# Kernel tuning notes

Hardware: AMD Instinct MI355X
Metric: run time of the kernel (lower is better)

The kernel has to match this reference:

```python
import jax, jax.numpy as jnp
import numpy as np

# Model dims (mamba-2.8b-ish layer, single 8192-token prefill)
H, I, N, R, K, L = 2048, 4096, 16, 128, 4, 8192


def setup_inputs() -> dict:
    key = jax.random.key(0)
    ks = jax.random.split(key, 7)
    return {
        "hidden_states": jax.random.normal(ks[0], (L, H), jnp.float32),
        "W_in": jax.random.normal(ks[1], (H, 2 * I), jnp.float32) * 0.02,   # in_proj (no bias)
        "conv_w": jax.random.normal(ks[2], (I, K), jnp.float32) * 0.2,      # depthwise conv weight
        "conv_b": jnp.zeros((I,), jnp.float32),                              # use_conv_bias=True
        "W_x": jax.random.normal(ks[3], (I, R + 2 * N), jnp.float32) * 0.02, # x_proj (no bias)
        "W_dt": jax.random.normal(ks[4], (R, I), jnp.float32) * 0.01,        # dt_proj weight
        "dt_bias": jax.random.normal(ks[5], (I,), jnp.float32) * 0.1,        # dt_proj bias (delta_bias)
        "A_log": jnp.log(jnp.broadcast_to(jnp.arange(1, N + 1, dtype=jnp.float32), (I, N))) + 0.0,
        "D": jnp.ones((I,), jnp.float32),
        "W_out": jax.random.normal(ks[6], (I, H), jnp.float32) * 0.02,       # out_proj (no bias)
    }


def silu(x):
    return x * jax.nn.sigmoid(x)


def causal_dw_conv(x, w, b):
    # x: [L, I]; depthwise causal conv along time (padding K-1, left only)
    xt = x.T[None]  # [1, I, L] (NCW)
    y = jax.lax.conv_general_dilated(xt, w[:, None, :], (1,), [(K - 1, 0)],
                                     feature_group_count=I)  # [1, I, L]
    return y[0].T + b


def mamba_forward(hidden_states, W_in, conv_w, conv_b, W_x, W_dt, dt_bias, A_log, D, W_out):
    proj = hidden_states @ W_in                     # [L, 2I]
    x, gate = proj[:, :I], proj[:, I:]
    x = silu(causal_dw_conv(x, conv_w, conv_b))     # causal_conv1d_fn with silu
    ssm = x @ W_x                                   # [L, R+2N]
    dt_lr, B, C = ssm[:, :R], ssm[:, R:R + N], ssm[:, R + N:]
    delta = jax.nn.softplus(dt_lr @ W_dt + dt_bias) # delta_softplus=True with delta_bias
    A = -jnp.exp(A_log)                             # [I, N]

    def step(h, t):
        d_t, B_t, C_t, u_t = t                      # [I], [N], [N], [I]
        h = h * jnp.exp(d_t[:, None] * A) + (d_t * u_t)[:, None] * B_t[None, :]
        return h, h @ C_t                           # y_t: [I]

    h0 = jnp.zeros((I, N), jnp.float32)
    _, y = jax.lax.scan(step, h0, (delta, B, C, x)) # y: [L, I]
    y = (y + x * D) * silu(gate)                    # skip D*u and z-gating (selective_scan_fn)
    return y @ W_out                                # out_proj -> [L, H]


def reference(hidden_states, W_in, conv_w, conv_b, W_x, W_dt, dt_bias, A_log, D, W_out):
    return mamba_forward(hidden_states, W_in, conv_w, conv_b, W_x, W_dt, dt_bias, A_log, D, W_out)
```

## Files before the change

### kernel.cpp

```cpp
#include <hip/hip_runtime.h>
#include <cmath>
#include <stdint.h>

#define H_DIM 2048
#define I_DIM 4096
#define N_DIM 16
#define R_DIM 128
#define K_CONV 4
#define L_DIM 8192
#define LC 2048
#define NCHUNK (L_DIM / LC)
#define SEG 32
#define TSEG (LC / SEG)
#define IN_DIM (I_DIM * N_DIM)

typedef _Float16 f16x8 __attribute__((ext_vector_type(8)));
typedef _Float16 f16x4v __attribute__((ext_vector_type(4)));
typedef float    f32x4 __attribute__((ext_vector_type(4)));

__device__ __forceinline__ void gl_lds(const _Float16* g, _Float16* lbase, int lane) {
#if __has_builtin(__builtin_amdgcn_global_load_lds)
    __builtin_amdgcn_global_load_lds(
        (const __attribute__((address_space(1))) void*)g,
        (__attribute__((address_space(3))) void*)lbase, 16, 0, 0);
#else
    *(f16x8*)&lbase[lane * 8] = *(const f16x8*)g;
#endif
}

template <int OUTF16>
__global__ __launch_bounds__(512, 1) void gemm_p256(
    const _Float16* __restrict__ Aph,
    const _Float16* __restrict__ Bph,
    void* __restrict__ Cv, int ldc, int Kd, int gm,
    int kchunk, size_t partStride)
{
    __shared__ __align__(16) _Float16 Sh[3][2][8192];

    const int tid = threadIdx.x;
    int bid = blockIdx.x;
    const int q = gridDim.x >> 3;
    bid = (bid & 7) * q + (bid >> 3);
    const int m0 = (bid % gm) * 256;
    const int n0 = (bid / gm) * 256;

    const int kbeg = blockIdx.y * kchunk;

    const int w = tid >> 6, l = tid & 63;
    const int wm = w & 3, wn = w >> 2;
    const int lr = l & 15, lg = l >> 4;

    const int KP = Kd >> 5;
    const int np0 = n0 >> 4, mp0 = m0 >> 4;
    const int st0 = w;

    f32x4 acc[4][8];
#pragma unroll
    for (int a = 0; a < 4; ++a)
#pragma unroll
        for (int b = 0; b < 8; ++b) acc[a][b] = (f32x4){0.f, 0.f, 0.f, 0.f};

    auto stage = [&](int k0, int p) {
        const int kp = k0 >> 5;
#pragma unroll
        for (int s = 0; s < 2; ++s) {
            const int st = st0 + s * 8;
            gl_lds(Aph + ((size_t)(mp0 + st) * KP + kp) * 512 + (size_t)l * 8,
                   &Sh[p][0][st * 512], l);
            gl_lds(Bph + ((size_t)(np0 + st) * KP + kp) * 512 + (size_t)l * 8,
                   &Sh[p][1][st * 512], l);
        }
    };
    auto domfma = [&](int b) {
        f16x8 fah[4];
#pragma unroll
        for (int t = 0; t < 4; ++t)
            fah[t] = *(const f16x8*)&Sh[b][0][(wm * 4 + t) * 512 + l * 8];
        __builtin_amdgcn_s_setprio(1);
#pragma unroll
        for (int nh = 0; nh < 2; ++nh) {
            f16x8 fbh[4];
#pragma unroll
            for (int t = 0; t < 4; ++t)
                fbh[t] = *(const f16x8*)&Sh[b][1][(wn * 8 + nh * 4 + t) * 512 + l * 8];
#pragma unroll
            for (int mt = 0; mt < 4; ++mt)
#pragma unroll
                for (int nt = 0; nt < 4; ++nt)
                    acc[mt][nh * 4 + nt] = __builtin_amdgcn_mfma_f32_16x16x32_f16(
                        fah[mt], fbh[nt], acc[mt][nh * 4 + nt], 0, 0, 0);
        }
        __builtin_amdgcn_s_setprio(0);
    };

    const int KT = kchunk >> 5;
    stage(kbeg, 0);
    stage(kbeg + 32, 1);
    for (int k = 0; k + 2 < KT; ++k) {
        stage(kbeg + (k + 2) * 32, (k + 2) % 3);
        asm volatile("s_waitcnt vmcnt(8)" ::: "memory");
        __builtin_amdgcn_s_barrier();
        __builtin_amdgcn_sched_barrier(0);
        domfma(k % 3);
        __builtin_amdgcn_s_barrier();
    }
    asm volatile("s_waitcnt vmcnt(4)" ::: "memory");
    __builtin_amdgcn_s_barrier();
    __builtin_amdgcn_sched_barrier(0);
    domfma((KT - 2) % 3);
    __builtin_amdgcn_s_barrier();
    asm volatile("s_waitcnt vmcnt(0)" ::: "memory");
    __builtin_amdgcn_s_barrier();
    __builtin_amdgcn_sched_barrier(0);
    domfma((KT - 1) % 3);

#pragma unroll
    for (int mt = 0; mt < 4; ++mt) {
        const int row = m0 + wm * 64 + mt * 16 + lg * 4;
#pragma unroll
        for (int nt = 0; nt < 8; ++nt) {
            const int col = n0 + wn * 128 + nt * 16 + lr;
#pragma unroll
            for (int j = 0; j < 4; ++j) {
                if (OUTF16) {
                    _Float16* C = (_Float16*)Cv + (size_t)blockIdx.y * partStride;
                    C[(size_t)(row + j) * ldc + col] = (_Float16)acc[mt][nt][j];
                } else {
                    float* C = (float*)Cv + (size_t)blockIdx.y * partStride;
                    C[(size_t)(row + j) * ldc + col] = acc[mt][nt][j];
                }
            }
        }
    }
}

__global__ __launch_bounds__(256) void reduce4_f16_kernel(
    const _Float16* __restrict__ P, float* __restrict__ out)
{
    const size_t idx = ((size_t)blockIdx.x * 256 + threadIdx.x) * 8;
    const size_t S = (size_t)LC * H_DIM;
    const f16x8 a = *(const f16x8*)(P + idx);
    const f16x8 b = *(const f16x8*)(P + S + idx);
    const f16x8 c = *(const f16x8*)(P + 2 * S + idx);
    const f16x8 d = *(const f16x8*)(P + 3 * S + idx);
    float r[8];
#pragma unroll
    for (int j = 0; j < 8; ++j)
        r[j] = ((float)a[j] + (float)b[j]) + ((float)c[j] + (float)d[j]);
    *(float4*)(out + idx)     = *(float4*)&r[0];
    *(float4*)(out + idx + 4) = *(float4*)&r[4];
}

template <int EPI, int AK, int ASPLIT, int BSPLIT, bool ATOMIC, int OUTF16>
__global__ __launch_bounds__(256, ASPLIT ? 2 : (BSPLIT ? 3 : 4)) void gemm_p(
    const void* __restrict__ Av, int lda,
    const _Float16* __restrict__ Aph,
    const _Float16* __restrict__ Bph, const _Float16* __restrict__ Bpl,
    void* __restrict__ Cv, int ldc,
    int Kd, int Ncap, int gm, int kchunk,
    const float* __restrict__ bias)
{
    constexpr int S_AH = 0;
    constexpr int S_AL = ASPLIT ? 1 : 0;
    constexpr int S_BH = ASPLIT ? 2 : 1;
    constexpr int S_BL = S_BH + 1;
    constexpr int NSLOT = S_BH + 1 + BSPLIT;
    __shared__ __align__(16) _Float16 Sh[2][NSLOT][4096];

    const int tid = threadIdx.x;
    int bid = blockIdx.x;
    const int q = gridDim.x >> 3;
    bid = (bid & 7) * q + (bid >> 3);
    const int m0 = (bid % gm) * 128;
    const int n0 = (bid / gm) * 128;

    const int kbeg = blockIdx.y * kchunk;
    const int kend = (kbeg + kchunk < Kd) ? (kbeg + kchunk) : Kd;

    const int w = tid >> 6, l = tid & 63;
    const int wm = w & 1, wn = w >> 1;
    const int lr = l & 15, lg = l >> 4;

    const int ar = tid >> 1, ah = tid & 1;
    const int aw0 = (ar >> 4) * 512 + (((ah * 2) * 16 + (ar & 15)) * 8);
    const int aw1 = aw0 + 128;

    const int KP = Kd >> 5;
    const int np0 = n0 >> 4;
    const int mp0 = m0 >> 4;

    f32x4 acc[4][4];
#pragma unroll
    for (int a = 0; a < 4; ++a)
#pragma unroll
        for (int b = 0; b < 4; ++b) acc[a][b] = (f32x4){0.f, 0.f, 0.f, 0.f};

    float xf[16];
    f16x8 sah[2], sal[2];

    auto issueA = [&](int k0) {
        if (AK == 0) {
            const float* Ap = (const float*)Av + (size_t)(m0 + ar) * lda + k0 + ah * 16;
            *(float4*)&xf[0]  = *(const float4*)(Ap + 0);
            *(float4*)&xf[4]  = *(const float4*)(Ap + 4);
            *(float4*)&xf[8]  = *(const float4*)(Ap + 8);
            *(float4*)&xf[12] = *(const float4*)(Ap + 12);
        }
    };
    auto cvtA = [&]() {
        if (AK == 0) {
#pragma unroll
            for (int c2 = 0; c2 < 2; ++c2)
#pragma unroll
                for (int j = 0; j < 8; ++j) {
                    const float xv = xf[c2 * 8 + j];
                    const _Float16 h = (_Float16)xv;
                    sah[c2][j] = h;
                    if (ASPLIT) sal[c2][j] = (_Float16)(xv - (float)h);
                }
        }
    };
    auto writeA = [&](int p) {
        *(f16x8*)&Sh[p][S_AH][aw0] = sah[0];
        *(f16x8*)&Sh[p][S_AH][aw1] = sah[1];
        if (ASPLIT) {
            *(f16x8*)&Sh[p][S_AL][aw0] = sal[0];
            *(f16x8*)&Sh[p][S_AL][aw1] = sal[1];
        }
    };
    auto stageGL = [&](int k0, int p) {
        const int kp = k0 >> 5;
        if (AK == 2) {
#pragma unroll
            for (int s = 0; s < 2; ++s) {
                const int st = w + s * 4;
                const size_t ga = ((size_t)(mp0 + st) * KP + kp) * 512 + (size_t)l * 8;
                gl_lds(Aph + ga, &Sh[p][S_AH][st * 512], l);
            }
        }
#pragma unroll
        for (int qq = 0; qq < 2; ++qq) {
            const int st = 2 * w + qq;
            const size_t go = ((size_t)(np0 + st) * KP + kp) * 512 + (size_t)l * 8;
            gl_lds(Bph + go, &Sh[p][S_BH][st * 512], l);
            if (BSPLIT) gl_lds(Bpl + go, &Sh[p][S_BL][st * 512], l);
        }
    };
    auto domfma = [&](int b) {
        f16x8 fah[4], fal[4], fbh[4], fbl[4];
#pragma unroll
        for (int t = 0; t < 4; ++t) {
            fah[t] = *(const f16x8*)&Sh[b][S_AH][(wm * 4 + t) * 512 + l * 8];
            if (ASPLIT) fal[t] = *(const f16x8*)&Sh[b][S_AL][(wm * 4 + t) * 512 + l * 8];
            fbh[t] = *(const f16x8*)&Sh[b][S_BH][(wn * 4 + t) * 512 + l * 8];
            if (BSPLIT) fbl[t] = *(const f16x8*)&Sh[b][S_BL][(wn * 4 + t) * 512 + l * 8];
        }
        __builtin_amdgcn_s_setprio(1);
#pragma unroll
        for (int mt = 0; mt < 4; ++mt)
#pragma unroll
            for (int nt = 0; nt < 4; ++nt) {
                f32x4& a = acc[mt][nt];
                a = __builtin_amdgcn_mfma_f32_16x16x32_f16(fah[mt], fbh[nt], a, 0, 0, 0);
                if (BSPLIT)
                    a = __builtin_amdgcn_mfma_f32_16x16x32_f16(fah[mt], fbl[nt], a, 0, 0, 0);
                if (ASPLIT)
                    a = __builtin_amdgcn_mfma_f32_16x16x32_f16(fal[mt], fbh[nt], a, 0, 0, 0);
            }
        __builtin_amdgcn_s_setprio(0);
    };

    if (AK != 2) { issueA(kbeg); cvtA(); writeA(0); }
    stageGL(kbeg, 0);
    __syncthreads();
    int p = 0;
    for (int k0 = kbeg; k0 < kend; k0 += 32) {
        const bool more = (k0 + 32 < kend);
        if (more) {
            if (AK != 2) issueA(k0 + 32);
            stageGL(k0 + 32, p ^ 1);
        }
        domfma(p);
        if (more && AK != 2) { cvtA(); writeA(p ^ 1); }
        __syncthreads();
        p ^= 1;
    }

#pragma unroll
    for (int mt = 0; mt < 4; ++mt) {
        const int row = m0 + wm * 64 + mt * 16 + lg * 4;
#pragma unroll
        for (int nt = 0; nt < 4; ++nt) {
            const int col = n0 + wn * 64 + nt * 16 + lr;
            if (Ncap == 0 || col < Ncap) {
#pragma unroll
                for (int j = 0; j < 4; ++j) {
                    float v = acc[mt][nt][j];
                    if (EPI == 1) {
                        v += bias[col];
                        v = (v > 20.f) ? v : __logf(1.f + __expf(v));
                    }
                    const size_t off = (size_t)(row + j) * ldc + col;
                    if (ATOMIC)      atomicAdd(&((float*)Cv)[off], v);
                    else if (OUTF16) ((_Float16*)Cv)[off] = (_Float16)v;
                    else             ((float*)Cv)[off] = v;
                }
            }
        }
    }
}

__global__ __launch_bounds__(128) void pack_bp(
    const float* __restrict__ W, _Float16* __restrict__ Ph,
    _Float16* __restrict__ Pl, int Kd, int Nd)
{
    __shared__ float t[32][33];
    const int tid = threadIdx.x;
    const int n0 = blockIdx.x * 32, k0 = blockIdx.y * 32;
#pragma unroll
    for (int h = 0; h < 2; ++h) {
        const int qd = tid + h * 128;
        const int kk = qd >> 3, qq = qd & 7;
        *(float4*)&t[kk][qq * 4] = *(const float4*)(W + (size_t)(k0 + kk) * Nd + n0 + qq * 4);
    }
    __syncthreads();
    const int c = tid >> 5, nn = tid & 31;
    const int np = (n0 + nn) >> 4;
    const int r  = nn & 15;
    const int kp = k0 >> 5;
    const size_t base = ((size_t)np * (Kd >> 5) + kp) * 512 + (c * 16 + r) * 8;
    f16x8 vh, vl;
#pragma unroll
    for (int j = 0; j < 8; ++j) {
        const float v = t[c * 8 + j][nn];
        const _Float16 h = (_Float16)v;
        vh[j] = h;
        vl[j] = (_Float16)(v - (float)h);
    }
    *(f16x8*)&Ph[base] = vh;
    if (Pl) *(f16x8*)&Pl[base] = vl;
}

__global__ __launch_bounds__(256) void pack_ap(
    const float* __restrict__ A, int lda,
    _Float16* __restrict__ Ph, int Kd)
{
    const int tid = threadIdx.x;
    const int mp = blockIdx.x;
    const int r = tid >> 4, c8 = tid & 15;
    const int k0 = blockIdx.y * 128 + c8 * 8;
    const float* Ap = A + (size_t)(mp * 16 + r) * lda + k0;
    const float4 v0 = *(const float4*)Ap;
    const float4 v1 = *(const float4*)(Ap + 4);
    const float x[8] = {v0.x, v0.y, v0.z, v0.w, v1.x, v1.y, v1.z, v1.w};
    f16x8 vh;
#pragma unroll
    for (int j = 0; j < 8; ++j) vh[j] = (_Float16)x[j];
    const int kp = k0 >> 5;
    const int c  = (k0 >> 3) & 3;
    const size_t base = ((size_t)mp * (Kd >> 5) + kp) * 512 + (c * 16 + r) * 8;
    *(f16x8*)&Ph[base] = vh;
}

__global__ __launch_bounds__(256) void conv_silu_kernel(
    const _Float16* __restrict__ proj,
    const float* __restrict__ xtail_in,
    float* __restrict__ xtail_out,
    const float* __restrict__ w,
    const float* __restrict__ b,
    float* __restrict__ xconv,
    float* __restrict__ ssm,
    int first)
{
    const int gid = blockIdx.x * 256 + threadIdx.x;
    if (gid < (LC * 160) / 4)
        *(float4*)(ssm + (size_t)gid * 4) = make_float4(0.f, 0.f, 0.f, 0.f);

    const int i4 = gid & (I_DIM / 4 - 1);
    const int t8 = gid >> 10;
    const int i = i4 * 4;
    const int tt0 = t8 * 8;

    const float4 w0 = *(const float4*)(w + (size_t)(i + 0) * 4);
    const float4 w1 = *(const float4*)(w + (size_t)(i + 1) * 4);
    const float4 w2 = *(const float4*)(w + (size_t)(i + 2) * 4);
    const float4 w3 = *(const float4*)(w + (size_t)(i + 3) * 4);
    const float4 bb = *(const float4*)(b + i);

    auto ldrow = [&](int row) -> float4 {
        const f16x4v v = *(const f16x4v*)(proj + (size_t)row * (2 * I_DIM) + i);
        return make_float4((float)v[0], (float)v[1], (float)v[2], (float)v[3]);
    };

    float4 r[11];
    if (tt0 >= 3) {
#pragma unroll
        for (int s = 0; s < 11; ++s) r[s] = ldrow(tt0 - 3 + s);
    } else {
#pragma unroll
        for (int s = 0; s < 3; ++s)
            r[s] = first ? make_float4(0.f, 0.f, 0.f, 0.f)
                         : *(const float4*)(xtail_in + (size_t)s * I_DIM + i);
#pragma unroll
        for (int s = 3; s < 11; ++s) r[s] = ldrow(tt0 - 3 + s);
    }

#pragma unroll
    for (int s = 0; s < 8; ++s) {
        float4 y = bb;
        y.x = fmaf(w0.x, r[s].x, y.x); y.x = fmaf(w0.y, r[s+1].x, y.x);
        y.x = fmaf(w0.z, r[s+2].x, y.x); y.x = fmaf(w0.w, r[s+3].x, y.x);
        y.y = fmaf(w1.x, r[s].y, y.y); y.y = fmaf(w1.y, r[s+1].y, y.y);
        y.y = fmaf(w1.z, r[s+2].y, y.y); y.y = fmaf(w1.w, r[s+3].y, y.y);
        y.z = fmaf(w2.x, r[s].z, y.z); y.z = fmaf(w2.y, r[s+1].z, y.z);
        y.z = fmaf(w2.z, r[s+2].z, y.z); y.z = fmaf(w2.w, r[s+3].z, y.z);
        y.w = fmaf(w3.x, r[s].w, y.w); y.w = fmaf(w3.y, r[s+1].w, y.w);
        y.w = fmaf(w3.z, r[s+2].w, y.w); y.w = fmaf(w3.w, r[s+3].w, y.w);
        y.x = y.x / (1.f + __expf(-y.x));
        y.y = y.y / (1.f + __expf(-y.y));
        y.z = y.z / (1.f + __expf(-y.z));
        y.w = y.w / (1.f + __expf(-y.w));
        *(float4*)(xconv + (size_t)(tt0 + s) * I_DIM + i) = y;
    }

    if (tt0 == LC - 8) {
#pragma unroll
        for (int qq = 0; qq < 3; ++qq)
            *(float4*)(xtail_out + (size_t)qq * I_DIM + i) = r[8 + qq];
    }
}

__global__ __launch_bounds__(256) void scan_part1(
    const _Float16* __restrict__ delta,
    const float* __restrict__ ssm,
    const float* __restrict__ xc,
    const float* __restrict__ A_log,
    float* __restrict__ aprod,
    float* __restrict__ hend)
{
    __shared__ float Bs[TSEG][16];
    const int tid = threadIdx.x;
    const int i = blockIdx.x * 128 + (tid >> 1);
    const int half = tid & 1;
    const int seg = blockIdx.y;
    const int t0 = seg * TSEG;

    {
        const int tt = tid >> 2, c = (tid & 3) * 4;
        *(float4*)&Bs[tt][c] = *(const float4*)&ssm[(size_t)(t0 + tt) * 160 + 128 + c];
    }
    __syncthreads();

    float Ai[8], h[8], ap[8];
    {
        const float4 a0 = *(const float4*)&A_log[(size_t)i * 16 + half * 8];
        const float4 a1 = *(const float4*)&A_log[(size_t)i * 16 + half * 8 + 4];
        const float al[8] = {a0.x, a0.y, a0.z, a0.w, a1.x, a1.y, a1.z, a1.w};
#pragma unroll
        for (int n = 0; n < 8; ++n) { Ai[n] = -expf(al[n]); h[n] = 0.f; ap[n] = 1.f; }
    }

    float d0 = (float)delta[(size_t)t0 * (2 * I_DIM) + i];
    float u0 = xc[(size_t)t0 * I_DIM + i];
    float d1 = (float)delta[(size_t)(t0 + 1) * (2 * I_DIM) + i];
    float u1 = xc[(size_t)(t0 + 1) * I_DIM + i];
    for (int t = 0; t < TSEG; t += 2) {
        float d2 = 0.f, u2 = 0.f, d3 = 0.f, u3 = 0.f;
        if (t + 3 < TSEG) {
            d2 = (float)delta[(size_t)(t0 + t + 2) * (2 * I_DIM) + i];
            u2 = xc[(size_t)(t0 + t + 2) * I_DIM + i];
            d3 = (float)delta[(size_t)(t0 + t + 3) * (2 * I_DIM) + i];
            u3 = xc[(size_t)(t0 + t + 3) * I_DIM + i];
        }
        {
            const float du = d0 * u0;
#pragma unroll
            for (int n = 0; n < 8; ++n) {
                const float a = __expf(d0 * Ai[n]);
                h[n] = fmaf(h[n], a, du * Bs[t][half * 8 + n]);
                ap[n] *= a;
            }
        }
        {
            const float du = d1 * u1;
#pragma unroll
            for (int n = 0; n < 8; ++n) {
                const float a = __expf(d1 * Ai[n]);
                h[n] = fmaf(h[n], a, du * Bs[t + 1][half * 8 + n]);
                ap[n] *= a;
            }
        }
        d0 = d2; u0 = u2; d1 = d3; u1 = u3;
    }

    const size_t base = (size_t)seg * IN_DIM + (size_t)i * 16 + half * 8;
#pragma unroll
    for (int qq = 0; qq < 2; ++qq) {
        float4 va = {ap[qq * 4 + 0], ap[qq * 4 + 1], ap[qq * 4 + 2], ap[qq * 4 + 3]};
        float4 vh = {h[qq * 4 + 0], h[qq * 4 + 1], h[qq * 4 + 2], h[qq * 4 + 3]};
        *(float4*)&aprod[base + qq * 4] = va;
        *(float4*)&hend[base + qq * 4]  = vh;
    }
}

__global__ __launch_bounds__(256) void scan_part2(
    const float* __restrict__ aprod,
    float* __restrict__ hend,
    float* __restrict__ hstate,
    int first)
{
    const int gid = blockIdx.x * 256 + threadIdx.x;
    float h = first ? 0.f : hstate[gid];
    for (int s = 0; s < SEG; ++s) {
        const int idx = s * IN_DIM + gid;
        const float ap = aprod[idx];
        const float he = hend[idx];
        hend[idx] = h;
        h = fmaf(ap, h, he);
    }
    hstate[gid] = h;
}

__global__ __launch_bounds__(256) void scan_part3(
    const _Float16* __restrict__ delta,
    const _Float16* __restrict__ gate,
    const float* __restrict__ ssm,
    const float* __restrict__ xc,
    _Float16* __restrict__ zPh,
    const float* __restrict__ A_log,
    const float* __restrict__ Dp,
    const float* __restrict__ hstart)
{
    __shared__ float BCs[TSEG][32];
    const int tid = threadIdx.x;
    const int i = blockIdx.x * 128 + (tid >> 1);
    const int half = tid & 1;
    const int seg = blockIdx.y;
    const int t0 = seg * TSEG;

    {
        const int tt = tid >> 2, c = (tid & 3) * 8;
        *(float4*)&BCs[tt][c]     = *(const float4*)&ssm[(size_t)(t0 + tt) * 160 + 128 + c];
        *(float4*)&BCs[tt][c + 4] = *(const float4*)&ssm[(size_t)(t0 + tt) * 160 + 132 + c];
    }
    __syncthreads();

    float Ai[8], h[8];
    {
        const float4 a0 = *(const float4*)&A_log[(size_t)i * 16 + half * 8];
        const float4 a1 = *(const float4*)&A_log[(size_t)i * 16 + half * 8 + 4];
        const float al[8] = {a0.x, a0.y, a0.z, a0.w, a1.x, a1.y, a1.z, a1.w};
#pragma unroll
        for (int n = 0; n < 8; ++n) Ai[n] = -expf(al[n]);
        const size_t base = (size_t)seg * IN_DIM + (size_t)i * 16 + half * 8;
        const float4 h0 = *(const float4*)&hstart[base];
        const float4 h1 = *(const float4*)&hstart[base + 4];
        h[0] = h0.x; h[1] = h0.y; h[2] = h0.z; h[3] = h0.w;
        h[4] = h1.x; h[5] = h1.y; h[6] = h1.z; h[7] = h1.w;
    }
    const float Di = Dp[i];

    const int kp = i >> 5, cc = (i >> 3) & 3, jj = i & 7;
    const size_t zb = (size_t)kp * 512 + (size_t)cc * 128 + jj;

    float d0 = (float)delta[(size_t)t0 * (2 * I_DIM) + i];
    float u0 = xc[(size_t)t0 * I_DIM + i];
    float g0 = (float)gate[(size_t)t0 * (2 * I_DIM) + i];
    float d1 = (float)delta[(size_t)(t0 + 1) * (2 * I_DIM) + i];
    float u1 = xc[(size_t)(t0 + 1) * I_DIM + i];
    float g1 = (float)gate[(size_t)(t0 + 1) * (2 * I_DIM) + i];
    for (int t = 0; t < TSEG; t += 2) {
        float d2 = 0.f, u2 = 0.f, g2 = 0.f, d3 = 0.f, u3 = 0.f, g3 = 0.f;
        if (t + 3 < TSEG) {
            d2 = (float)delta[(size_t)(t0 + t + 2) * (2 * I_DIM) + i];
            u2 = xc[(size_t)(t0 + t + 2) * I_DIM + i];
            g2 = (float)gate[(size_t)(t0 + t + 2) * (2 * I_DIM) + i];
            d3 = (float)delta[(size_t)(t0 + t + 3) * (2 * I_DIM) + i];
            u3 = xc[(size_t)(t0 + t + 3) * I_DIM + i];
            g3 = (float)gate[(size_t)(t0 + t + 3) * (2 * I_DIM) + i];
        }
#pragma unroll
        for (int ss = 0; ss < 2; ++ss) {
            const float d = ss ? d1 : d0;
            const float u = ss ? u1 : u0;
            const float g = ss ? g1 : g0;
            const int tt = t + ss;
            const float du = d * u;
            float y = 0.f;
#pragma unroll
            for (int n = 0; n < 8; ++n) {
                const float a = __expf(d * Ai[n]);
                h[n] = fmaf(h[n], a, du * BCs[tt][half * 8 + n]);
                y = fmaf(h[n], BCs[tt][16 + half * 8 + n], y);
            }
            y += __shfl_xor(y, 1);
            if (half == 0) {
                const float sg = g / (1.f + __expf(-g));
                const float zv = (y + u * Di) * sg;
                const int row = t0 + tt;
                zPh[((size_t)(row >> 4) * (I_DIM >> 5)) * 512 + zb + (size_t)(row & 15) * 8]
                    = (_Float16)zv;
            }
        }
        d0 = d2; u0 = u2; g0 = g2; d1 = d3; u1 = u3; g1 = g3;
    }
}

extern "C" void kernel_launch(void* const* d_in, const int* in_sizes, int n_in,
                              void* d_out, int out_size, void* d_ws, size_t ws_size,
                              hipStream_t stream)
{
    const float* hs      = (const float*)d_in[0];
    const float* W_in    = (const float*)d_in[1];
    const float* conv_w  = (const float*)d_in[2];
    const float* conv_b  = (const float*)d_in[3];
    const float* W_x     = (const float*)d_in[4];
    const float* W_dt    = (const float*)d_in[5];
    const float* dt_bias = (const float*)d_in[6];
    const float* A_log   = (const float*)d_in[7];
    const float* Dp      = (const float*)d_in[8];
    const float* W_out   = (const float*)d_in[9];
    float* out = (float*)d_out;

    char* p = (char*)d_ws;
    auto alloc = [&](size_t bytes) {
        char* r = p;
        p += (bytes + 255) & ~(size_t)255;
        return r;
    };
    _Float16* proj16 = (_Float16*)alloc((size_t)36 * 1024 * 1024);
    float* xconv  = (float*)alloc((size_t)LC * I_DIM * 4);
    float* ssm    = (float*)alloc((size_t)LC * 160 * 4);
    float* xtail  = (float*)alloc((size_t)2 * 3 * I_DIM * 4);
    float* hstate = (float*)alloc((size_t)IN_DIM * 4);
    _Float16* WinPh  = (_Float16*)alloc((size_t)2 * I_DIM * H_DIM * 2);
    _Float16* WoutPh = (_Float16*)alloc((size_t)H_DIM * I_DIM * 2);
    _Float16* WdtPh  = (_Float16*)alloc((size_t)I_DIM * R_DIM * 2);
    _Float16* WdtPl  = (_Float16*)alloc((size_t)I_DIM * R_DIM * 2);
    _Float16* WxPh   = (_Float16*)alloc((size_t)256 * I_DIM * 2);
    _Float16* WxPl   = (_Float16*)alloc((size_t)256 * I_DIM * 2);
    _Float16* hsPh   = (_Float16*)alloc((size_t)L_DIM * H_DIM * 2);
    _Float16* zPh    = (_Float16*)alloc((size_t)LC * I_DIM * 2);

    const dim3 blk(256);
    const int NSSM = R_DIM + 2 * N_DIM;

    pack_bp<<<dim3(2 * I_DIM / 32, H_DIM / 32), dim3(128), 0, stream>>>(
        W_in, WinPh, nullptr, H_DIM, 2 * I_DIM);
    pack_bp<<<dim3(H_DIM / 32, I_DIM / 32), dim3(128), 0, stream>>>(
        W_out, WoutPh, nullptr, I_DIM, H_DIM);
    pack_bp<<<dim3(I_DIM / 32, R_DIM / 32), dim3(128), 0, stream>>>(
        W_dt, WdtPh, WdtPl, R_DIM, I_DIM);
    pack_bp<<<dim3(NSSM / 32, I_DIM / 32), dim3(128), 0, stream>>>(
        W_x, WxPh, WxPl, I_DIM, NSSM);
    pack_ap<<<dim3(L_DIM / 16, H_DIM / 128), blk, 0, stream>>>(
        hs, H_DIM, hsPh, H_DIM);

    for (int c = 0; c < NCHUNK; ++c) {
        const int t0 = c * LC;
        const int first = (c == 0) ? 1 : 0;
        float* out_c = out + (size_t)t0 * H_DIM;
        float* aprod = out_c;
        float* hend  = out_c + (size_t)SEG * IN_DIM;
        float* xtA = xtail + (size_t)(c & 1) * 3 * I_DIM;
        float* xtB = xtail + (size_t)((c & 1) ^ 1) * 3 * I_DIM;
        const _Float16* hsPh_c = hsPh + (size_t)(t0 >> 4) * (H_DIM >> 5) * 512;

        gemm_p256<1><<<dim3(256, 1), dim3(512), 0, stream>>>(
            hsPh_c, WinPh, proj16, 2 * I_DIM, H_DIM, LC / 256, H_DIM, 0);

        conv_silu_kernel<<<dim3(1024), blk, 0, stream>>>(
            proj16, xtA, xtB, conv_w, conv_b, xconv, ssm, first);

        gemm_p<0, 0, 1, 1, true, 0><<<dim3(32, 8), blk, 0, stream>>>(
            xconv, I_DIM, nullptr, WxPh, WxPl, ssm, NSSM,
            I_DIM, NSSM, LC / 128, I_DIM / 8, nullptr);

        gemm_p<1, 0, 1, 1, false, 1><<<dim3(512, 1), blk, 0, stream>>>(
            ssm, NSSM, nullptr, WdtPh, WdtPl, proj16, 2 * I_DIM,
            R_DIM, 0, LC / 128, R_DIM, dt_bias);

        scan_part1<<<dim3(I_DIM / 128, SEG), blk, 0, stream>>>(
            proj16, ssm, xconv, A_log, aprod, hend);
        scan_part2<<<dim3(IN_DIM / 256), blk, 0, stream>>>(
            aprod, hend, hstate, first);
        scan_part3<<<dim3(I_DIM / 128, SEG), blk, 0, stream>>>(
            proj16, proj16 + I_DIM, ssm, xconv, zPh, A_log, Dp, hend);

        gemm_p256<1><<<dim3(64, 4), dim3(512), 0, stream>>>(
            zPh, WoutPh, proj16, H_DIM, I_DIM, H_DIM / 256,
            I_DIM / 4, (size_t)LC * H_DIM);

        reduce4_f16_kernel<<<dim3(LC * H_DIM / 2048), blk, 0, stream>>>(
            proj16, out_c);
    }
}
```

Measured before the change: 1.071 ms.

## Rework 256x256 GEMM to 4 waves loading A directly into registers

Cuts the large-tile GEMM from 8 to 4 waves, each computing a 128x128 sub-tile (8x8 MFMA accumulators). The A operand is now loaded straight from global memory into registers, double-buffered across two register sets, and only B is staged through LDS with a triple buffer. The goals are less LDS traffic and LDS footprint, and more MFMA work per wave so fewer fragment loads are needed per MFMA. In exchange, register pressure rises sharply (256 accumulator floats plus 16 A fragments per lane), which risks spills, and latency hiding from other waves drops.

```diff
diff --git a/kernel.cpp b/kernel.cpp
--- a/kernel.cpp
+++ b/kernel.cpp
@@ -29,13 +29,13 @@
 }
 
 template <int OUTF16>
-__global__ __launch_bounds__(512, 1) void gemm_p256(
+__global__ __launch_bounds__(256, 1) void gemm_q256(
     const _Float16* __restrict__ Aph,
     const _Float16* __restrict__ Bph,
     void* __restrict__ Cv, int ldc, int Kd, int gm,
     int kchunk, size_t partStride)
 {
-    __shared__ __align__(16) _Float16 Sh[3][2][8192];
+    __shared__ __align__(16) _Float16 Bs[3][8192];
 
     const int tid = threadIdx.x;
     int bid = blockIdx.x;
@@ -43,80 +43,92 @@
     bid = (bid & 7) * q + (bid >> 3);
     const int m0 = (bid % gm) * 256;
     const int n0 = (bid / gm) * 256;
-
     const int kbeg = blockIdx.y * kchunk;
 
     const int w = tid >> 6, l = tid & 63;
-    const int wm = w & 3, wn = w >> 2;
+    const int wm = w & 1, wn = w >> 1;
     const int lr = l & 15, lg = l >> 4;
 
     const int KP = Kd >> 5;
     const int np0 = n0 >> 4, mp0 = m0 >> 4;
-    const int st0 = w;
-
-    f32x4 acc[4][8];
-#pragma unroll
-    for (int a = 0; a < 4; ++a)
+
+    f32x4 acc[8][8];
+#pragma unroll
+    for (int a = 0; a < 8; ++a)
 #pragma unroll
         for (int b = 0; b < 8; ++b) acc[a][b] = (f32x4){0.f, 0.f, 0.f, 0.f};
 
-    auto stage = [&](int k0, int p) {
+    const _Float16* Abase = Aph + ((size_t)(mp0 + wm * 8) * KP) * 512 + (size_t)l * 8;
+    const size_t Astride = (size_t)KP * 512;
+
+    auto loadA = [&](int k0, f16x8* fa) {
+        const size_t ko = (size_t)(k0 >> 5) * 512;
+#pragma unroll
+        for (int mt = 0; mt < 8; ++mt)
+            fa[mt] = *(const f16x8*)(Abase + (size_t)mt * Astride + ko);
+    };
+    auto stageB = [&](int k0, int p) {
         const int kp = k0 >> 5;
 #pragma unroll
-        for (int s = 0; s < 2; ++s) {
-            const int st = st0 + s * 8;
-            gl_lds(Aph + ((size_t)(mp0 + st) * KP + kp) * 512 + (size_t)l * 8,
-                   &Sh[p][0][st * 512], l);
+        for (int s = 0; s < 4; ++s) {
+            const int st = w * 4 + s;
             gl_lds(Bph + ((size_t)(np0 + st) * KP + kp) * 512 + (size_t)l * 8,
-                   &Sh[p][1][st * 512], l);
-        }
-    };
-    auto domfma = [&](int b) {
-        f16x8 fah[4];
-#pragma unroll
-        for (int t = 0; t < 4; ++t)
-            fah[t] = *(const f16x8*)&Sh[b][0][(wm * 4 + t) * 512 + l * 8];
+                   &Bs[p][st * 512], l);
+        }
+    };
+    auto domfma = [&](int p, f16x8* fa) {
+        f16x8 fb[8];
+#pragma unroll
+        for (int nt = 0; nt < 8; ++nt)
+            fb[nt] = *(const f16x8*)&Bs[p][(wn * 8 + nt) * 512 + l * 8];
         __builtin_amdgcn_s_setprio(1);
 #pragma unroll
-        for (int nh = 0; nh < 2; ++nh) {
-            f16x8 fbh[4];
-#pragma unroll
-            for (int t = 0; t < 4; ++t)
-                fbh[t] = *(const f16x8*)&Sh[b][1][(wn * 8 + nh * 4 + t) * 512 + l * 8];
-#pragma unroll
-            for (int mt = 0; mt < 4; ++mt)
-#pragma unroll
-                for (int nt = 0; nt < 4; ++nt)
-                    acc[mt][nh * 4 + nt] = __builtin_amdgcn_mfma_f32_16x16x32_f16(
-                        fah[mt], fbh[nt], acc[mt][nh * 4 + nt], 0, 0, 0);
-        }
+        for (int mt = 0; mt < 8; ++mt)
+#pragma unroll
+            for (int nt = 0; nt < 8; ++nt)
+                acc[mt][nt] = __builtin_amdgcn_mfma_f32_16x16x32_f16(
+                    fa[mt], fb[nt], acc[mt][nt], 0, 0, 0);
         __builtin_amdgcn_s_setprio(0);
     };
 
+    f16x8 faA[8], faB[8];
     const int KT = kchunk >> 5;
-    stage(kbeg, 0);
-    stage(kbeg + 32, 1);
-    for (int k = 0; k + 2 < KT; ++k) {
-        stage(kbeg + (k + 2) * 32, (k + 2) % 3);
-        asm volatile("s_waitcnt vmcnt(8)" ::: "memory");
+
+    stageB(kbeg, 0);
+    stageB(kbeg + 32, 1);
+    loadA(kbeg, faA);
+
+    int k = 0;
+    for (; k + 3 < KT; k += 2) {
+        stageB(kbeg + (k + 2) * 32, (k + 2) % 3);
+        loadA(kbeg + (k + 1) * 32, faB);
+        asm volatile("s_waitcnt vmcnt(12)" ::: "memory");
         __builtin_amdgcn_s_barrier();
         __builtin_amdgcn_sched_barrier(0);
-        domfma(k % 3);
+        domfma(k % 3, faA);
         __builtin_amdgcn_s_barrier();
-    }
-    asm volatile("s_waitcnt vmcnt(4)" ::: "memory");
+        stageB(kbeg + (k + 3) * 32, (k + 3) % 3);
+        loadA(kbeg + (k + 2) * 32, faA);
+        asm volatile("s_waitcnt vmcnt(12)" ::: "memory");
+        __builtin_amdgcn_s_barrier();
+        __builtin_amdgcn_sched_barrier(0);
+        domfma((k + 1) % 3, faB);
+        __builtin_amdgcn_s_barrier();
+    }
+    loadA(kbeg + (KT - 1) * 32, faB);
+    asm volatile("s_waitcnt vmcnt(8)" ::: "memory");
     __builtin_amdgcn_s_barrier();
     __builtin_amdgcn_sched_barrier(0);
-    domfma((KT - 2) % 3);
+    domfma((KT - 2) % 3, faA);
     __builtin_amdgcn_s_barrier();
     asm volatile("s_waitcnt vmcnt(0)" ::: "memory");
     __builtin_amdgcn_s_barrier();
     __builtin_amdgcn_sched_barrier(0);
-    domfma((KT - 1) % 3);
-
-#pragma unroll
-    for (int mt = 0; mt < 4; ++mt) {
-        const int row = m0 + wm * 64 + mt * 16 + lg * 4;
+    domfma((KT - 1) % 3, faB);
+
+#pragma unroll
+    for (int mt = 0; mt < 8; ++mt) {
+        const int row = m0 + wm * 128 + mt * 16 + lg * 4;
 #pragma unroll
         for (int nt = 0; nt < 8; ++nt) {
             const int col = n0 + wn * 128 + nt * 16 + lr;
@@ -666,7 +678,7 @@
         float* xtB = xtail + (size_t)((c & 1) ^ 1) * 3 * I_DIM;
         const _Float16* hsPh_c = hsPh + (size_t)(t0 >> 4) * (H_DIM >> 5) * 512;
 
-        gemm_p256<1><<<dim3(256, 1), dim3(512), 0, stream>>>(
+        gemm_q256<1><<<dim3(256, 1), blk, 0, stream>>>(
             hsPh_c, WinPh, proj16, 2 * I_DIM, H_DIM, LC / 256, H_DIM, 0);
 
         conv_silu_kernel<<<dim3(1024), blk, 0, stream>>>(
@@ -687,7 +699,7 @@
         scan_part3<<<dim3(I_DIM / 128, SEG), blk, 0, stream>>>(
             proj16, proj16 + I_DIM, ssm, xconv, zPh, A_log, Dp, hend);
 
-        gemm_p256<1><<<dim3(64, 4), dim3(512), 0, stream>>>(
+        gemm_q256<1><<<dim3(64, 4), blk, 0, stream>>>(
             zPh, WoutPh, proj16, H_DIM, I_DIM, H_DIM / 256,
             I_DIM / 4, (size_t)LC * H_DIM);
 
```

Result: slower. 1.125 ms (+5.1%).
